# Performance work log

Measured on AMD Instinct MI355X. Metric: run time of the kernel, lower is better.

The kernel has to match this reference:

```python
import jax, jax.numpy as jnp
from jax import lax
import numpy as np

N = 10000      # num_nodes
T = 24         # hist_len
IN_DIM = 16
HID = 128
HEADS = 4
E = 160000     # num_edges
PRED = 24
NEG_SLOPE = 0.2  # GATv2 LeakyReLU default


def _lstm_layer(xs, wih, whh, bih, bhh):
    # xs: [T, N, D]; PyTorch gate order i, f, g, o
    Hh = whh.shape[1]
    h0 = jnp.zeros((xs.shape[1], Hh), xs.dtype)
    def step(carry, xt):
        h, c = carry
        g = xt @ wih.T + bih + h @ whh.T + bhh
        i, f, gg, o = jnp.split(g, 4, axis=-1)
        c = jax.nn.sigmoid(f) * c + jax.nn.sigmoid(i) * jnp.tanh(gg)
        h = jax.nn.sigmoid(o) * jnp.tanh(c)
        return (h, c), h
    (_, _), out = lax.scan(step, (h0, h0), xs)
    return out  # [T, N, Hh]


def _gatv2(z, src, dst, wl, bl, wr, br, att, bias):
    # PyG GATv2Conv: share_weights=False, concat=True, add_self_loops=False
    n = z.shape[0]
    xl = (z @ wl.T + bl).reshape(n, HEADS, HID)   # source/message transform
    xr = (z @ wr.T + br).reshape(n, HEADS, HID)   # target transform
    e = jax.nn.leaky_relu(xl[src] + xr[dst], NEG_SLOPE)   # [E, H, C]
    score = jnp.einsum('ehc,hc->eh', e, att)              # [E, H]
    smax = jax.ops.segment_max(score, dst, num_segments=n)
    p = jnp.exp(score - smax[dst])
    denom = jax.ops.segment_sum(p, dst, num_segments=n)
    alpha = p / (denom[dst] + 1e-16)                      # segment softmax over in-edges
    out = jax.ops.segment_sum(xl[src] * alpha[:, :, None], dst, num_segments=n)
    return out.reshape(n, HEADS * HID) + bias


def setup_inputs() -> dict:
    key = jax.random.key(0)
    ks = iter(jax.random.split(key, 64))
    def W(shape):
        return jax.random.normal(next(ks), shape, jnp.float32) / np.sqrt(shape[-1])
    inp = {}
    inp['x'] = jax.random.normal(next(ks), (N, T, IN_DIM), jnp.float32)
    inp['edge_index'] = jax.random.randint(next(ks), (2, E), 0, N, jnp.int32)
    inp['mlp_in_w0'] = W((HID, IN_DIM)); inp['mlp_in_b0'] = jnp.zeros((HID,), jnp.float32)
    inp['mlp_in_w1'] = W((HID, HID));    inp['mlp_in_b1'] = jnp.zeros((HID,), jnp.float32)
    for l in range(2):  # nn.LSTM(num_layers = lstm_num_layers*2 = 2)
        inp[f'lstm_wih{l}'] = W((4 * HID, HID))
        inp[f'lstm_whh{l}'] = W((4 * HID, HID))
        inp[f'lstm_bih{l}'] = jnp.zeros((4 * HID,), jnp.float32)
        inp[f'lstm_bhh{l}'] = jnp.zeros((4 * HID,), jnp.float32)
    for l in range(2):  # nGAT_layer = 2
        inp[f'gat{l}_wl'] = W((HEADS * HID, HID))
        inp[f'gat{l}_bl'] = jnp.zeros((HEADS * HID,), jnp.float32)
        inp[f'gat{l}_wr'] = W((HEADS * HID, HID))
        inp[f'gat{l}_br'] = jnp.zeros((HEADS * HID,), jnp.float32)
        inp[f'gat{l}_att'] = W((HEADS, HID))
        inp[f'gat{l}_bias'] = jnp.zeros((HEADS * HID,), jnp.float32)
        inp[f'gat{l}_pw'] = W((HID, HEADS * HID))
        inp[f'gat{l}_pb'] = jnp.zeros((HID,), jnp.float32)
    inp['mlp_out_w0'] = W((HID, HID));  inp['mlp_out_b0'] = jnp.zeros((HID,), jnp.float32)
    inp['mlp_out_w1'] = W((PRED, HID)); inp['mlp_out_b1'] = jnp.zeros((PRED,), jnp.float32)
    return inp


def _forward(x, edge_index, mlp_in_w0, mlp_in_b0, mlp_in_w1, mlp_in_b1,
             lstm_wih0, lstm_whh0, lstm_bih0, lstm_bhh0,
             lstm_wih1, lstm_whh1, lstm_bih1, lstm_bhh1,
             gat0_wl, gat0_bl, gat0_wr, gat0_br, gat0_att, gat0_bias, gat0_pw, gat0_pb,
             gat1_wl, gat1_bl, gat1_wr, gat1_br, gat1_att, gat1_bias, gat1_pw, gat1_pb,
             mlp_out_w0, mlp_out_b0, mlp_out_w1, mlp_out_b1):
    src, dst = edge_index[0], edge_index[1]
    h = jnp.transpose(x, (1, 0, 2))                       # [T, N, in_dim]
    # MLP_layers_in: Linear(in,hid), Linear(hid,hid), ReLU
    h = h @ mlp_in_w0.T + mlp_in_b0
    h = jax.nn.relu(h @ mlp_in_w1.T + mlp_in_b1)
    # 2-layer unidirectional LSTM
    h = _lstm_layer(h, lstm_wih0, lstm_whh0, lstm_bih0, lstm_bhh0)
    h = _lstm_layer(h, lstm_wih1, lstm_whh1, lstm_bih1, lstm_bhh1)
    z = h[-1]                                             # [N, HID] last timestep
    # GAT block x2: GATv2Conv -> Linear(heads*hid, hid) -> ReLU
    z = _gatv2(z, src, dst, gat0_wl, gat0_bl, gat0_wr, gat0_br, gat0_att, gat0_bias)
    z = jax.nn.relu(z @ gat0_pw.T + gat0_pb)
    z = _gatv2(z, src, dst, gat1_wl, gat1_bl, gat1_wr, gat1_br, gat1_att, gat1_bias)
    z = jax.nn.relu(z @ gat1_pw.T + gat1_pb)
    # MLP_layers_out: Linear(hid,hid), ReLU, Linear(hid, pred_len)
    z = jax.nn.relu(z @ mlp_out_w0.T + mlp_out_b0)
    return z @ mlp_out_w1.T + mlp_out_b1                  # [N, PRED]


def reference(x, edge_index, mlp_in_w0, mlp_in_b0, mlp_in_w1, mlp_in_b1,
              lstm_wih0, lstm_whh0, lstm_bih0, lstm_bhh0,
              lstm_wih1, lstm_whh1, lstm_bih1, lstm_bhh1,
              gat0_wl, gat0_bl, gat0_wr, gat0_br, gat0_att, gat0_bias, gat0_pw, gat0_pb,
              gat1_wl, gat1_bl, gat1_wr, gat1_br, gat1_att, gat1_bias, gat1_pw, gat1_pb,
              mlp_out_w0, mlp_out_b0, mlp_out_w1, mlp_out_b1):
    return _forward(x, edge_index, mlp_in_w0, mlp_in_b0, mlp_in_w1, mlp_in_b1,
                    lstm_wih0, lstm_whh0, lstm_bih0, lstm_bhh0,
                    lstm_wih1, lstm_whh1, lstm_bih1, lstm_bhh1,
                    gat0_wl, gat0_bl, gat0_wr, gat0_br, gat0_att, gat0_bias, gat0_pw, gat0_pb,
                    gat1_wl, gat1_bl, gat1_wr, gat1_br, gat1_att, gat1_bias, gat1_pw, gat1_pb,
                    mlp_out_w0, mlp_out_b0, mlp_out_w1, mlp_out_b1)
```

## Files before the change

kernel.cpp:

```cpp
#include <hip/hip_runtime.h>
#include <hip/hip_bf16.h>

#define NNODES 10000
#define TLEN 24
#define INDIM 16
#define HID 128
#define GDIM 512

typedef __hip_bfloat16 bf16;
typedef short v8s __attribute__((ext_vector_type(8)));
typedef float v4f __attribute__((ext_vector_type(4)));

__device__ inline float u2f(unsigned u){ return __uint_as_float(u); }
__device__ inline float frcp(float x){ return __builtin_amdgcn_rcpf(x); }

__device__ inline void unpack8(uint4 v, float* f){
  f[0]=u2f(v.x<<16); f[1]=u2f(v.x&0xFFFF0000u);
  f[2]=u2f(v.y<<16); f[3]=u2f(v.y&0xFFFF0000u);
  f[4]=u2f(v.z<<16); f[5]=u2f(v.z&0xFFFF0000u);
  f[6]=u2f(v.w<<16); f[7]=u2f(v.w&0xFFFF0000u);
}

__global__ __launch_bounds__(256) void conv_w_k(
    const float* s0, const float* s1, const float* s2, const float* s3,
    const float* s4, const float* s5, const float* s6, const float* s7,
    const float* s8, const float* s9, const float* s10,
    bf16* __restrict__ dst, int* __restrict__ deg)
{
  int idx = blockIdx.x*256 + threadIdx.x;
  if (idx < NNODES) deg[idx] = 0;
  if (idx >= 671744) return;
  int c = idx >> 16;
  float v;
  if (c < 10){
    const float* srcs[10] = {s0,s1,s2,s3,s4,s5,s6,s7,s8,s9};
    v = srcs[c][idx & 0xFFFF];
  } else {
    v = s10[idx - 655360];
  }
  dst[idx] = __float2bfloat16(v);
}

__global__ __launch_bounds__(256) void prep_w_k(
    const float* __restrict__ miw0, const float* __restrict__ mib0,
    const float* __restrict__ miw1, const float* __restrict__ mib1,
    const float* __restrict__ bih0, const float* __restrict__ bhh0,
    const float* __restrict__ bih1, const float* __restrict__ bhh1,
    const float* __restrict__ bl0, const float* __restrict__ br0,
    const float* __restrict__ bl1, const float* __restrict__ br1,
    float* __restrict__ Wp, float* __restrict__ bp,
    float* __restrict__ bsum, float* __restrict__ gblr)
{
  int t = threadIdx.x;
  int b = blockIdx.x;
  if (b < 8){
    int idx = b*256 + t;
    int j = idx >> 4, d = idx & 15;
    float s = 0.f;
    for (int k=0;k<HID;k++) s += miw1[j*HID+k] * miw0[k*INDIM+d];
    Wp[idx] = s;
    return;
  }
  if (t < HID){
    float s = mib1[t];
    for (int k=0;k<HID;k++) s += miw1[t*HID+k] * mib0[k];
    bp[t] = s;
  }
  for (int i = t; i < GDIM; i += 256){
    bsum[i]        = bih0[i] + bhh0[i];
    bsum[GDIM + i] = bih1[i] + bhh1[i];
  }
  for (int i = t; i < GDIM; i += 256){
    gblr[i]          = bl0[i];
    gblr[GDIM + i]   = br0[i];
    gblr[1024 + i]   = bl1[i];
    gblr[1536 + i]   = br1[i];
  }
}

__global__ __launch_bounds__(256) void mlp_in_k(
    const float* __restrict__ x, const float* __restrict__ Wp,
    const float* __restrict__ bp, bf16* __restrict__ X0)
{
  __shared__ __align__(16) float xs[64*16];
  const int tid = threadIdx.x;
  const int m0 = blockIdx.x*64;
  {
    int row = tid >> 2, q = tid & 3;
    int m = m0 + row;
    int t = m / NNODES, n = m - t*NNODES;
    float4 v = *(const float4*)(x + ((size_t)n*TLEN + t)*INDIM + q*4);
    *(float4*)(xs + row*16 + q*4) = v;
  }
  const int j = tid & 127;
  const int half = tid >> 7;
  const float* wr = Wp + j*INDIM;
  float4 w0 = *(const float4*)(wr);
  float4 w1 = *(const float4*)(wr + 4);
  float4 w2 = *(const float4*)(wr + 8);
  float4 w3 = *(const float4*)(wr + 12);
  float bj = bp[j];
  __syncthreads();
  #pragma unroll 4
  for (int mi=0; mi<32; mi++){
    int row = mi*2 + half;
    const float* xr = xs + row*16;
    float4 a0 = *(const float4*)(xr);
    float4 a1 = *(const float4*)(xr + 4);
    float4 a2 = *(const float4*)(xr + 8);
    float4 a3 = *(const float4*)(xr + 12);
    float s = bj
      + a0.x*w0.x + a0.y*w0.y + a0.z*w0.z + a0.w*w0.w
      + a1.x*w1.x + a1.y*w1.y + a1.z*w1.z + a1.w*w1.w
      + a2.x*w2.x + a2.y*w2.y + a2.z*w2.z + a2.w*w2.w
      + a3.x*w3.x + a3.y*w3.y + a3.z*w3.z + a3.w*w3.w;
    s = s > 0.f ? s : 0.f;
    X0[(size_t)(m0+row)*HID + j] = __float2bfloat16(s);
  }
}

template<int WRITE_ALL>
__global__ __launch_bounds__(1024) void lstm_cs(
    const bf16* __restrict__ Xin, const bf16* __restrict__ Wih,
    const bf16* __restrict__ Whh, const float* __restrict__ bias,
    bf16* __restrict__ out)
{
  __shared__ __align__(16) float gs[48*516];
  __shared__ __align__(16) bf16 xs[48*136];
  __shared__ __align__(16) bf16 hb[48*136];
  const int tid = threadIdx.x;
  const int w = tid >> 6;
  const int lane = tid & 63;
  const int r16 = lane & 15, quad = lane >> 4;
  const int m0 = blockIdx.x*48;

  v8s wbi[2][4], wbh[2][4];
  #pragma unroll
  for (int ct=0; ct<2; ct++)
    #pragma unroll
    for (int kc=0; kc<4; kc++){
      size_t o = (size_t)(w*32 + ct*16 + r16)*HID + kc*32 + quad*8;
      wbi[ct][kc] = *(const v8s*)(Wih + o);
      wbh[ct][kc] = *(const v8s*)(Whh + o);
    }
  const float bw0 = bias[w*32 + r16];
  const float bw1 = bias[w*32 + 16 + r16];

  const int srow = tid >> 4;
  const int c8   = (tid & 15) * 8;
  const int gr   = m0 + srow;
  const int grc  = gr < NNODES ? gr : NNODES-1;
  const size_t TS = (size_t)NNODES*HID;
  const bf16* ldp = Xin + (size_t)grc*HID + c8;
  bf16* stp = (bf16*)Xin + (size_t)gr*HID + c8;

  for (int i = tid; i < 816; i += 1024)
    ((uint4*)hb)[i] = make_uint4(0,0,0,0);
  if (tid < 768)
    *(uint4*)(xs + srow*136 + c8) = *(const uint4*)ldp;
  __syncthreads();

  float c[3][2];
  #pragma unroll
  for (int rt=0; rt<3; rt++){ c[rt][0] = 0.f; c[rt][1] = 0.f; }

  const int fb = r16*136 + quad*8;

  #pragma unroll 1
  for (int t=0; t<TLEN; t++){
    uint4 xa;
    if (tid < 768){
      int tn = t+1 < TLEN ? t+1 : TLEN-1;
      xa = *(const uint4*)(ldp + (size_t)tn*TS);
      if (WRITE_ALL && t > 0 && gr < NNODES)
        *(uint4*)(stp + (size_t)(t-1)*TS) = *(const uint4*)(hb + srow*136 + c8);
    }
    #pragma unroll
    for (int rt=0; rt<3; rt++){
      v4f a0 = (v4f)0.f, a1 = (v4f)0.f;
      #pragma unroll
      for (int kc=0; kc<4; kc++){
        v8s av = *(const v8s*)(xs + rt*2176 + fb + kc*32);
        a0 = __builtin_amdgcn_mfma_f32_16x16x32_bf16(av, wbi[0][kc], a0, 0, 0, 0);
        a1 = __builtin_amdgcn_mfma_f32_16x16x32_bf16(av, wbi[1][kc], a1, 0, 0, 0);
      }
      #pragma unroll
      for (int kc=0; kc<4; kc++){
        v8s hv = *(const v8s*)(hb + rt*2176 + fb + kc*32);
        a0 = __builtin_amdgcn_mfma_f32_16x16x32_bf16(hv, wbh[0][kc], a0, 0, 0, 0);
        a1 = __builtin_amdgcn_mfma_f32_16x16x32_bf16(hv, wbh[1][kc], a1, 0, 0, 0);
      }
      int gwb = (rt*16 + quad*4)*516 + w*32 + r16;
      #pragma unroll
      for (int r=0; r<4; r++){
        gs[gwb + r*516]      = a0[r] + bw0;
        gs[gwb + r*516 + 16] = a1[r] + bw1;
      }
    }
    __syncthreads();
    #pragma unroll
    for (int rt=0; rt<3; rt++){
      const int erow = rt*16 + w;
      const float* grd = gs + erow*516 + 2*lane;
      float2 gi = *(const float2*)(grd);
      float2 gf = *(const float2*)(grd + 128);
      float2 gg = *(const float2*)(grd + 256);
      float2 go = *(const float2*)(grd + 384);
      unsigned short hu[2];
      #pragma unroll
      for (int j=0; j<2; j++){
        float iv = j ? gi.y : gi.x;
        float fv = j ? gf.y : gf.x;
        float gv = j ? gg.y : gg.x;
        float ov = j ? go.y : go.x;
        float sf = frcp(1.f + __expf(-fv));
        float ei = __expf(-iv);
        float tg = __expf(-2.f*fabsf(gv));
        float itg = copysignf((1.f - tg)*frcp((1.f + ei)*(1.f + tg)), gv);
        float cn = sf*c[rt][j] + itg;
        c[rt][j] = cn;
        float eo = __expf(-ov);
        float tc = __expf(-2.f*fabsf(cn));
        float hh = copysignf((1.f - tc)*frcp((1.f + eo)*(1.f + tc)), cn);
        __hip_bfloat16 hv16 = __float2bfloat16(hh);
        hu[j] = *reinterpret_cast<unsigned short*>(&hv16);
      }
      *(unsigned*)(hb + erow*136 + 2*lane) = ((unsigned)hu[1] << 16) | hu[0];
    }
    if (tid < 768)
      *(uint4*)(xs + srow*136 + c8) = xa;
    __syncthreads();
  }

  if (tid < 768 && gr < NNODES){
    uint4 h = *(const uint4*)(hb + srow*136 + c8);
    if (WRITE_ALL) *(uint4*)(stp + (size_t)(TLEN-1)*TS) = h;
    else           *(uint4*)(out + (size_t)gr*HID + c8) = h;
  }
}

template<int ACT>
__global__ __launch_bounds__(256) void gemm_bt(
    const bf16* __restrict__ A, const bf16* __restrict__ B,
    const float* __restrict__ bias, bf16* __restrict__ C,
    int M, int N, int K)
{
  __shared__ __align__(16) bf16 As[128*40];
  __shared__ __align__(16) bf16 Bs[128*40];
  const int tid = threadIdx.x;
  const int m0 = blockIdx.x*128, n0 = blockIdx.y*128;
  const int lane = tid & 63, wave = tid >> 6;
  const int r16 = lane & 15, quad = lane >> 4;

  v4f acc[2][8];
  #pragma unroll
  for (int a=0;a<2;a++)
    #pragma unroll
    for (int b=0;b<8;b++) acc[a][b] = (v4f)0.f;

  for (int k0=0; k0<K; k0+=32){
    #pragma unroll
    for (int i=0;i<2;i++){
      int li = tid + i*256;
      int row = li >> 2, q4 = li & 3;
      uint4 va = make_uint4(0,0,0,0);
      int gm = m0 + row;
      if (gm < M) va = *(const uint4*)(A + (size_t)gm*K + k0 + q4*8);
      *(uint4*)(As + row*40 + q4*8) = va;
      uint4 vb = make_uint4(0,0,0,0);
      int gn = n0 + row;
      if (gn < N) vb = *(const uint4*)(B + (size_t)gn*K + k0 + q4*8);
      *(uint4*)(Bs + row*40 + q4*8) = vb;
    }
    __syncthreads();
    v8s av[2], bv[8];
    #pragma unroll
    for (int mi=0;mi<2;mi++)
      av[mi] = *(const v8s*)(As + (wave*32 + mi*16 + r16)*40 + quad*8);
    #pragma unroll
    for (int ni=0;ni<8;ni++)
      bv[ni] = *(const v8s*)(Bs + (ni*16 + r16)*40 + quad*8);
    #pragma unroll
    for (int mi=0;mi<2;mi++)
      #pragma unroll
      for (int ni=0;ni<8;ni++)
        acc[mi][ni] = __builtin_amdgcn_mfma_f32_16x16x32_bf16(av[mi], bv[ni], acc[mi][ni], 0, 0, 0);
    __syncthreads();
  }

  #pragma unroll
  for (int mi=0;mi<2;mi++){
    #pragma unroll
    for (int r=0;r<4;r++){
      int row = m0 + wave*32 + mi*16 + quad*4 + r;
      if (row >= M) continue;
      #pragma unroll
      for (int ni=0;ni<8;ni++){
        int col = n0 + ni*16 + r16;
        float v = acc[mi][ni][r] + bias[col];
        if (ACT == 1) v = v > 0.f ? v : 0.f;
        C[(size_t)row*N + col] = __float2bfloat16(v);
      }
    }
  }
}

template<int ACT>
__global__ __launch_bounds__(256) void gemm_bt64(
    const bf16* __restrict__ A, const bf16* __restrict__ B,
    const float* __restrict__ bias, bf16* __restrict__ C,
    int M, int K)
{
  __shared__ __align__(16) bf16 As[64*40];
  __shared__ __align__(16) bf16 Bs[128*40];
  const int tid = threadIdx.x;
  const int m0 = blockIdx.x*64;
  const int lane = tid & 63, wave = tid >> 6;
  const int r16 = lane & 15, quad = lane >> 4;

  v4f acc[8];
  #pragma unroll
  for (int b=0;b<8;b++) acc[b] = (v4f)0.f;

  for (int k0=0; k0<K; k0+=32){
    {
      int row = tid >> 2, q4 = tid & 3;
      uint4 va = make_uint4(0,0,0,0);
      int gm = m0 + row;
      if (gm < M) va = *(const uint4*)(A + (size_t)gm*K + k0 + q4*8);
      *(uint4*)(As + row*40 + q4*8) = va;
    }
    #pragma unroll
    for (int i=0;i<2;i++){
      int li = tid + i*256;
      int row = li >> 2, q4 = li & 3;
      uint4 vb = *(const uint4*)(B + (size_t)row*K + k0 + q4*8);
      *(uint4*)(Bs + row*40 + q4*8) = vb;
    }
    __syncthreads();
    v8s av, bv[8];
    av = *(const v8s*)(As + (wave*16 + r16)*40 + quad*8);
    #pragma unroll
    for (int ni=0;ni<8;ni++)
      bv[ni] = *(const v8s*)(Bs + (ni*16 + r16)*40 + quad*8);
    #pragma unroll
    for (int ni=0;ni<8;ni++)
      acc[ni] = __builtin_amdgcn_mfma_f32_16x16x32_bf16(av, bv[ni], acc[ni], 0, 0, 0);
    __syncthreads();
  }

  #pragma unroll
  for (int r=0;r<4;r++){
    int row = m0 + wave*16 + quad*4 + r;
    if (row >= M) continue;
    #pragma unroll
    for (int ni=0;ni<8;ni++){
      int col = ni*16 + r16;
      float v = acc[ni][r] + bias[col];
      if (ACT == 1) v = v > 0.f ? v : 0.f;
      C[(size_t)row*HID + col] = __float2bfloat16(v);
    }
  }
}

__global__ __launch_bounds__(256) void mlp_out_fused_k(
    const bf16* __restrict__ A, const bf16* __restrict__ B,
    const float* __restrict__ bias, const float* __restrict__ w1,
    const float* __restrict__ b1, float* __restrict__ out, int M)
{
  __shared__ __align__(16) bf16 As[64*40];
  __shared__ __align__(16) bf16 Bs[128*40];
  __shared__ __align__(16) bf16 o0s[64*136];
  const int tid = threadIdx.x;
  const int m0 = blockIdx.x*64;
  const int lane = tid & 63, wave = tid >> 6;
  const int r16 = lane & 15, quad = lane >> 4;

  v4f acc[8];
  #pragma unroll
  for (int b=0;b<8;b++) acc[b] = (v4f)0.f;

  for (int k0=0; k0<HID; k0+=32){
    {
      int row = tid >> 2, q4 = tid & 3;
      uint4 va = make_uint4(0,0,0,0);
      int gm = m0 + row;
      if (gm < M) va = *(const uint4*)(A + (size_t)gm*HID + k0 + q4*8);
      *(uint4*)(As + row*40 + q4*8) = va;
    }
    #pragma unroll
    for (int i=0;i<2;i++){
      int li = tid + i*256;
      int row = li >> 2, q4 = li & 3;
      uint4 vb = *(const uint4*)(B + (size_t)row*HID + k0 + q4*8);
      *(uint4*)(Bs + row*40 + q4*8) = vb;
    }
    __syncthreads();
    v8s av, bv[8];
    av = *(const v8s*)(As + (wave*16 + r16)*40 + quad*8);
    #pragma unroll
    for (int ni=0;ni<8;ni++)
      bv[ni] = *(const v8s*)(Bs + (ni*16 + r16)*40 + quad*8);
    #pragma unroll
    for (int ni=0;ni<8;ni++)
      acc[ni] = __builtin_amdgcn_mfma_f32_16x16x32_bf16(av, bv[ni], acc[ni], 0, 0, 0);
    __syncthreads();
  }

  #pragma unroll
  for (int r=0;r<4;r++){
    int row = wave*16 + quad*4 + r;
    #pragma unroll
    for (int ni=0;ni<8;ni++){
      int col = ni*16 + r16;
      float v = acc[ni][r] + bias[col];
      v = v > 0.f ? v : 0.f;
      o0s[row*136 + col] = __float2bfloat16(v);
    }
  }
  __syncthreads();

  for (int idx = tid; idx < 64*24; idx += 256){
    int row = idx / 24, j = idx - row*24;
    if (m0 + row >= M) continue;
    const bf16* ar = o0s + row*136;
    const float* wr = w1 + j*HID;
    float s = b1[j];
    for (int k=0;k<HID;k+=8){
      float fa[8];
      unpack8(*(const uint4*)(ar+k), fa);
      float4 w0 = *(const float4*)(wr + k);
      float4 w1v = *(const float4*)(wr + k + 4);
      s += fa[0]*w0.x + fa[1]*w0.y + fa[2]*w0.z + fa[3]*w0.w
         + fa[4]*w1v.x + fa[5]*w1v.y + fa[6]*w1v.z + fa[7]*w1v.w;
    }
    out[(size_t)(m0+row)*24 + j] = s;
  }
}

__global__ void deg_count_k(const int* __restrict__ dst, int* __restrict__ deg, int E){
  int e = blockIdx.x*256 + threadIdx.x;
  if (e < E){
    unsigned d = (unsigned)dst[e];
    if (d < (unsigned)NNODES) atomicAdd(&deg[d], 1);
  }
}

__global__ void scan_k(const int* __restrict__ deg, int* __restrict__ offs,
                       int* __restrict__ cursor, int n)
{
  __shared__ int part[256];
  __shared__ int base[256];
  int t = threadIdx.x;
  int lo = t*40, hi = lo+40;
  if (lo > n) lo = n;
  if (hi > n) hi = n;
  int s = 0;
  for (int i=lo;i<hi;i++) s += deg[i];
  part[t] = s;
  __syncthreads();
  if (t == 0){
    int run=0;
    for (int i=0;i<256;i++){ base[i]=run; run+=part[i]; }
    offs[n] = run;
  }
  __syncthreads();
  int run = base[t];
  for (int i=lo;i<hi;i++){ offs[i]=run; cursor[i]=run; run += deg[i]; }
}

__global__ void fill_k(const int* __restrict__ src, const int* __restrict__ dst,
                       int* __restrict__ cursor, int* __restrict__ srcs, int E){
  int e = blockIdx.x*256 + threadIdx.x;
  if (e < E){
    unsigned d = (unsigned)dst[e];
    if (d < (unsigned)NNODES){
      int p = atomicAdd(&cursor[d], 1);
      unsigned s = (unsigned)src[e];
      srcs[p] = (s < (unsigned)NNODES) ? (int)s : 0;
    }
  }
}

__global__ __launch_bounds__(256) void gat_onl(
    const int* __restrict__ offs, const int* __restrict__ srcs,
    const bf16* __restrict__ xc, const float* __restrict__ att,
    const float* __restrict__ gbias, bf16* __restrict__ agg)
{
  int d = blockIdx.x*4 + (threadIdx.x >> 6);
  if (d >= NNODES) return;
  int lane = threadIdx.x & 63;
  float fr[8];
  unpack8(*(const uint4*)(xc + (size_t)d*1024 + 512 + lane*8), fr);
  float4 a0 = *(const float4*)(att + lane*8);
  float4 a1 = *(const float4*)(att + lane*8 + 4);
  float fa[8] = {a0.x,a0.y,a0.z,a0.w,a1.x,a1.y,a1.z,a1.w};
  int i0 = offs[d], i1 = offs[d+1];

  float m = -3.4e38f, den = 0.f;
  float acc[8] = {0,0,0,0,0,0,0,0};

  if (i0 < i1){
    uint4 r0 = *(const uint4*)(xc + (size_t)srcs[i0]*1024 + lane*8);
    uint4 r1 = r0;
    if (i0+1 < i1) r1 = *(const uint4*)(xc + (size_t)srcs[i0+1]*1024 + lane*8);
    for (int i=i0; i<i1; i++){
      uint4 r2 = r1;
      if (i+2 < i1) r2 = *(const uint4*)(xc + (size_t)srcs[i+2]*1024 + lane*8);
      float fl[8];
      unpack8(r0, fl);
      float p = 0.f;
      #pragma unroll
      for (int q=0;q<8;q++){
        float v = fl[q] + fr[q];
        v = v > 0.f ? v : 0.2f*v;
        p += v*fa[q];
      }
      p += __shfl_xor(p, 1); p += __shfl_xor(p, 2);
      p += __shfl_xor(p, 4); p += __shfl_xor(p, 8);
      float mn = fmaxf(m, p);
      float corr = __expf(m - mn);
      float w = __expf(p - mn);
      den = den*corr + w;
      #pragma unroll
      for (int q=0;q<8;q++) acc[q] = acc[q]*corr + w*fl[q];
      m = mn;
      r0 = r1; r1 = r2;
    }
  }
  float r = 1.f/(den + 1e-16f);
  float4 b0 = *(const float4*)(gbias + lane*8);
  float4 b1 = *(const float4*)(gbias + lane*8 + 4);
  float fb[8] = {b0.x,b0.y,b0.z,b0.w,b1.x,b1.y,b1.z,b1.w};
  #pragma unroll
  for (int q=0;q<8;q++)
    agg[(size_t)d*GDIM + lane*8 + q] = __float2bfloat16(acc[q]*r + fb[q]);
}


extern "C" void kernel_launch(void* const* d_in, const int* in_sizes, int n_in,
                              void* d_out, int out_size, void* d_ws, size_t ws_size,
                              hipStream_t stream)
{
  const float* x   = (const float*)d_in[0];
  const int*   ei  = (const int*)d_in[1];
  const int E = in_sizes[1] / 2;
  const int* srcp = ei;
  const int* dstp = ei + E;

  const float* miw0 = (const float*)d_in[2];
  const float* mib0 = (const float*)d_in[3];
  const float* miw1 = (const float*)d_in[4];
  const float* mib1 = (const float*)d_in[5];
  const float* wih0 = (const float*)d_in[6];
  const float* whh0 = (const float*)d_in[7];
  const float* bih0 = (const float*)d_in[8];
  const float* bhh0 = (const float*)d_in[9];
  const float* wih1 = (const float*)d_in[10];
  const float* whh1 = (const float*)d_in[11];
  const float* bih1 = (const float*)d_in[12];
  const float* bhh1 = (const float*)d_in[13];
  const float* g_wl[2]   = {(const float*)d_in[14], (const float*)d_in[22]};
  const float* g_bl[2]   = {(const float*)d_in[15], (const float*)d_in[23]};
  const float* g_wr[2]   = {(const float*)d_in[16], (const float*)d_in[24]};
  const float* g_br[2]   = {(const float*)d_in[17], (const float*)d_in[25]};
  const float* g_att[2]  = {(const float*)d_in[18], (const float*)d_in[26]};
  const float* g_bias[2] = {(const float*)d_in[19], (const float*)d_in[27]};
  const float* g_pw[2]   = {(const float*)d_in[20], (const float*)d_in[28]};
  const float* g_pb[2]   = {(const float*)d_in[21], (const float*)d_in[29]};
  const float* mow0 = (const float*)d_in[30];
  const float* mob0 = (const float*)d_in[31];
  const float* mow1 = (const float*)d_in[32];
  const float* mob1 = (const float*)d_in[33];
  (void)n_in; (void)out_size; (void)ws_size;

  char* base = (char*)d_ws;
  size_t off = 0;
  auto carve = [&](size_t n)->char*{
    char* p = base + off;
    off = (off + n + 255) & ~(size_t)255;
    return p;
  };
  char*  X0r = carve((size_t)TLEN*NNODES*HID*2);
  bf16*  zf  = (bf16*)carve((size_t)NNODES*HID*2);
  float* Wp  = (float*)carve(HID*INDIM*4);
  float* bp  = (float*)carve(HID*4);
  float* bsum= (float*)carve(2*GDIM*4);
  float* gblr= (float*)carve(2*1024*4);
  bf16*  wbf = (bf16*)carve((size_t)671744*2);
  int*   offsb = (int*)carve((size_t)(NNODES+1)*4);
  int*   curs  = (int*)carve((size_t)NNODES*4);
  int*   srcs  = (int*)carve((size_t)E*4);
  int*   deg   = (int*)carve((size_t)NNODES*4);
  bf16*  agg   = (bf16*)carve((size_t)NNODES*GDIM*2);

  const bf16* wih0b = wbf + 0;
  const bf16* whh0b = wbf + 65536;
  const bf16* wih1b = wbf + 131072;
  const bf16* whh1b = wbf + 196608;
  const bf16* wlr0b = wbf + 262144;
  const bf16* pw0b  = wbf + 393216;
  const bf16* wlr1b = wbf + 458752;
  const bf16* pw1b  = wbf + 589824;
  const bf16* mow0b = wbf + 655360;
  const bf16* wlrb[2] = {wlr0b, wlr1b};
  const bf16* pwb[2]  = {pw0b, pw1b};

  bf16* X0 = (bf16*)X0r;
  bf16* xc = (bf16*)X0r;
  bf16* z2 = (bf16*)(X0r + 20480000);
  bf16* z3 = (bf16*)(X0r + 23040000);

  conv_w_k<<<2624, 256, 0, stream>>>(wih0, whh0, wih1, whh1,
                                     g_wl[0], g_wr[0], g_pw[0],
                                     g_wl[1], g_wr[1], g_pw[1], mow0, wbf, deg);
  prep_w_k<<<9, 256, 0, stream>>>(miw0, mib0, miw1, mib1,
                                  bih0, bhh0, bih1, bhh1,
                                  g_bl[0], g_br[0], g_bl[1], g_br[1],
                                  Wp, bp, bsum, gblr);

  mlp_in_k<<<(TLEN*NNODES)/64, 256, 0, stream>>>(x, Wp, bp, X0);

  deg_count_k<<<(E+255)/256, 256, 0, stream>>>(dstp, deg, E);
  scan_k<<<1, 256, 0, stream>>>(deg, offsb, curs, NNODES);
  fill_k<<<(E+255)/256, 256, 0, stream>>>(srcp, dstp, curs, srcs, E);

  const int NBL48 = (NNODES + 47) / 48;
  lstm_cs<1><<<NBL48, 1024, 0, stream>>>(X0, wih0b, whh0b, bsum, nullptr);
  lstm_cs<0><<<NBL48, 1024, 0, stream>>>(X0, wih1b, whh1b, bsum + GDIM, zf);

  const bf16* zin = zf;
  bf16* zouts[2] = {z2, z3};
  const int NB64 = (NNODES + 63) / 64;
  for (int l=0; l<2; l++){
    gemm_bt<0><<<dim3(79,8), 256, 0, stream>>>(zin, wlrb[l], gblr + l*1024, xc, NNODES, 1024, HID);
    gat_onl<<<(NNODES+3)/4, 256, 0, stream>>>(offsb, srcs, xc, g_att[l], g_bias[l], agg);
    gemm_bt64<1><<<NB64, 256, 0, stream>>>(agg, pwb[l], g_pb[l], zouts[l], NNODES, GDIM);
    zin = zouts[l];
  }

  mlp_out_fused_k<<<NB64, 256, 0, stream>>>(z3, mow0b, mob0, mow1, mob1,
                                            (float*)d_out, NNODES);
}
```

Baseline: 559.8 us.

## Permute LSTM weight rows so gates stay in registers, double-buffer x/h

LSTM weight rows are reordered at conversion time so each wave's MFMA tiles hold all four gates (i,f,g,o) for the same hidden columns. Gate values are exchanged with a lane shuffle instead of a round trip through a large fp32 shared-memory gate buffer. This removes one block-wide barrier per timestep and shrinks LDS use. x and h tiles are double-buffered so the next step's inputs can be written without conflicting with current reads, at the cost of scattered 2-byte h stores to LDS.

```diff
diff --git a/kernel.cpp b/kernel.cpp
--- a/kernel.cpp
+++ b/kernel.cpp
@@ -32,7 +32,14 @@
   if (idx >= 671744) return;
   int c = idx >> 16;
   float v;
-  if (c < 10){
+  if (c < 4){
+    const float* srcs[4] = {s0,s1,s2,s3};
+    int m = idx & 0xFFFF;
+    int p = m >> 7, k = m & 127;
+    int wv = p >> 5, ct = (p >> 4) & 1, r = p & 15;
+    int orow = (ct*2 + (r>>3))*HID + wv*8 + (r&7);
+    v = srcs[c][orow*HID + k];
+  } else if (c < 10){
     const float* srcs[10] = {s0,s1,s2,s3,s4,s5,s6,s7,s8,s9};
     v = srcs[c][idx & 0xFFFF];
   } else {
@@ -120,18 +127,18 @@
 }
 
 template<int WRITE_ALL>
-__global__ __launch_bounds__(1024) void lstm_cs(
+__global__ __launch_bounds__(1024) void lstm_pk(
     const bf16* __restrict__ Xin, const bf16* __restrict__ Wih,
     const bf16* __restrict__ Whh, const float* __restrict__ bias,
     bf16* __restrict__ out)
 {
-  __shared__ __align__(16) float gs[48*516];
-  __shared__ __align__(16) bf16 xs[48*136];
-  __shared__ __align__(16) bf16 hb[48*136];
+  __shared__ __align__(16) bf16 xs[2][48*136];
+  __shared__ __align__(16) bf16 hs[2][48*136];
   const int tid = threadIdx.x;
   const int w = tid >> 6;
   const int lane = tid & 63;
   const int r16 = lane & 15, quad = lane >> 4;
+  const int side = r16 >> 3;
   const int m0 = blockIdx.x*48;
 
   v8s wbi[2][4], wbh[2][4];
@@ -143,8 +150,9 @@
       wbi[ct][kc] = *(const v8s*)(Wih + o);
       wbh[ct][kc] = *(const v8s*)(Whh + o);
     }
-  const float bw0 = bias[w*32 + r16];
-  const float bw1 = bias[w*32 + 16 + r16];
+  const int hc = w*8 + (r16 & 7);
+  const float bwi = bias[hc],       bwf = bias[HID + hc];
+  const float bwg = bias[2*HID+hc], bwo = bias[3*HID + hc];
 
   const int srow = tid >> 4;
   const int c8   = (tid & 15) * 8;
@@ -155,85 +163,81 @@
   bf16* stp = (bf16*)Xin + (size_t)gr*HID + c8;
 
   for (int i = tid; i < 816; i += 1024)
-    ((uint4*)hb)[i] = make_uint4(0,0,0,0);
+    ((uint4*)hs[0])[i] = make_uint4(0,0,0,0);
   if (tid < 768)
-    *(uint4*)(xs + srow*136 + c8) = *(const uint4*)ldp;
+    *(uint4*)(xs[0] + srow*136 + c8) = *(const uint4*)ldp;
   __syncthreads();
 
-  float c[3][2];
-  #pragma unroll
-  for (int rt=0; rt<3; rt++){ c[rt][0] = 0.f; c[rt][1] = 0.f; }
-
-  const int fb = r16*136 + quad*8;
+  float cst[3][2];
+  #pragma unroll
+  for (int rt=0; rt<3; rt++){ cst[rt][0] = 0.f; cst[rt][1] = 0.f; }
+
+  const int fb  = r16*136 + quad*8;
+  const int hwb = (quad*4 + side*2)*136 + hc;
 
   #pragma unroll 1
   for (int t=0; t<TLEN; t++){
+    const int cur = t & 1, nxt = cur ^ 1;
+    const bf16* xrd = xs[cur];
+    const bf16* hrd = hs[cur];
+    bf16* hwr = hs[nxt];
+
     uint4 xa;
     if (tid < 768){
       int tn = t+1 < TLEN ? t+1 : TLEN-1;
       xa = *(const uint4*)(ldp + (size_t)tn*TS);
       if (WRITE_ALL && t > 0 && gr < NNODES)
-        *(uint4*)(stp + (size_t)(t-1)*TS) = *(const uint4*)(hb + srow*136 + c8);
-    }
+        *(uint4*)(stp + (size_t)(t-1)*TS) = *(const uint4*)(hrd + srow*136 + c8);
+    }
+
     #pragma unroll
     for (int rt=0; rt<3; rt++){
       v4f a0 = (v4f)0.f, a1 = (v4f)0.f;
       #pragma unroll
       for (int kc=0; kc<4; kc++){
-        v8s av = *(const v8s*)(xs + rt*2176 + fb + kc*32);
+        v8s av = *(const v8s*)(xrd + rt*2176 + fb + kc*32);
         a0 = __builtin_amdgcn_mfma_f32_16x16x32_bf16(av, wbi[0][kc], a0, 0, 0, 0);
         a1 = __builtin_amdgcn_mfma_f32_16x16x32_bf16(av, wbi[1][kc], a1, 0, 0, 0);
       }
       #pragma unroll
       for (int kc=0; kc<4; kc++){
-        v8s hv = *(const v8s*)(hb + rt*2176 + fb + kc*32);
+        v8s hv = *(const v8s*)(hrd + rt*2176 + fb + kc*32);
         a0 = __builtin_amdgcn_mfma_f32_16x16x32_bf16(hv, wbh[0][kc], a0, 0, 0, 0);
         a1 = __builtin_amdgcn_mfma_f32_16x16x32_bf16(hv, wbh[1][kc], a1, 0, 0, 0);
       }
-      int gwb = (rt*16 + quad*4)*516 + w*32 + r16;
+      float p0[4], p1[4];
       #pragma unroll
       for (int r=0; r<4; r++){
-        gs[gwb + r*516]      = a0[r] + bw0;
-        gs[gwb + r*516 + 16] = a1[r] + bw1;
+        p0[r] = __shfl_xor(a0[r], 8);
+        p1[r] = __shfl_xor(a1[r], 8);
       }
-    }
-    __syncthreads();
-    #pragma unroll
-    for (int rt=0; rt<3; rt++){
-      const int erow = rt*16 + w;
-      const float* grd = gs + erow*516 + 2*lane;
-      float2 gi = *(const float2*)(grd);
-      float2 gf = *(const float2*)(grd + 128);
-      float2 gg = *(const float2*)(grd + 256);
-      float2 go = *(const float2*)(grd + 384);
-      unsigned short hu[2];
       #pragma unroll
       for (int j=0; j<2; j++){
-        float iv = j ? gi.y : gi.x;
-        float fv = j ? gf.y : gf.x;
-        float gv = j ? gg.y : gg.x;
-        float ov = j ? go.y : go.x;
+        float iv = (side ? p0[2+j] : a0[j]) + bwi;
+        float fv = (side ? a0[2+j] : p0[j]) + bwf;
+        float gv = (side ? p1[2+j] : a1[j]) + bwg;
+        float ov = (side ? a1[2+j] : p1[j]) + bwo;
         float sf = frcp(1.f + __expf(-fv));
         float ei = __expf(-iv);
         float tg = __expf(-2.f*fabsf(gv));
         float itg = copysignf((1.f - tg)*frcp((1.f + ei)*(1.f + tg)), gv);
-        float cn = sf*c[rt][j] + itg;
-        c[rt][j] = cn;
+        float cn = sf*cst[rt][j] + itg;
+        cst[rt][j] = cn;
         float eo = __expf(-ov);
         float tc = __expf(-2.f*fabsf(cn));
         float hh = copysignf((1.f - tc)*frcp((1.f + eo)*(1.f + tc)), cn);
-        __hip_bfloat16 hv16 = __float2bfloat16(hh);
-        hu[j] = *reinterpret_cast<unsigned short*>(&hv16);
+        hwr[rt*2176 + hwb + j*136] = __float2bfloat16(hh);
       }
-      *(unsigned*)(hb + erow*136 + 2*lane) = ((unsigned)hu[1] << 16) | hu[0];
-    }
+    }
+
     if (tid < 768)
-      *(uint4*)(xs + srow*136 + c8) = xa;
+      *(uint4*)(xs[nxt] + srow*136 + c8) = xa;
     __syncthreads();
   }
 
   if (tid < 768 && gr < NNODES){
-    uint4 h = *(const uint4*)(hb + srow*136 + c8);
+    const bf16* hf = hs[TLEN & 1];
+    uint4 h = *(const uint4*)(hf + srow*136 + c8);
     if (WRITE_ALL) *(uint4*)(stp + (size_t)(TLEN-1)*TS) = h;
     else           *(uint4*)(out + (size_t)gr*HID + c8) = h;
   }
@@ -626,8 +630,8 @@
   fill_k<<<(E+255)/256, 256, 0, stream>>>(srcp, dstp, curs, srcs, E);
 
   const int NBL48 = (NNODES + 47) / 48;
-  lstm_cs<1><<<NBL48, 1024, 0, stream>>>(X0, wih0b, whh0b, bsum, nullptr);
-  lstm_cs<0><<<NBL48, 1024, 0, stream>>>(X0, wih1b, whh1b, bsum + GDIM, zf);
+  lstm_pk<1><<<NBL48, 1024, 0, stream>>>(X0, wih0b, whh0b, bsum, nullptr);
+  lstm_pk<0><<<NBL48, 1024, 0, stream>>>(X0, wih1b, whh1b, bsum + GDIM, zf);
 
   const bf16* zin = zf;
   bf16* zouts[2] = {z2, z3};
```

Result: faster. 534.8 us (-4.5%).
